# Performance work log

Measured on AMD Instinct MI355X. Metric: run time of the kernel, lower is better.

## Reference

```python
import jax, jax.numpy as jnp
import numpy as np

SCALE = 32.0 / 32.0  # alpha / rank
KEEP = 1.0 - 0.05    # dropout keep prob


def setup_inputs() -> dict:
    key = jax.random.key(0)
    kx, kw, ka, kb, km = jax.random.split(key, 5)
    B_, S, D_in, D_out, R = 4, 2048, 4096, 4096, 32
    x = jax.random.normal(kx, (B_, S, D_in), dtype=jnp.float32)
    W = jax.random.normal(kw, (D_out, D_in), dtype=jnp.float32) * (1.0 / np.sqrt(D_in))
    A = jax.random.normal(ka, (D_in, R), dtype=jnp.float32) * (1.0 / np.sqrt(D_in))
    Bm = jax.random.normal(kb, (R, D_out), dtype=jnp.float32) * 0.02
    # deterministic inverted-dropout mask: {0, 1/KEEP}
    drop_mask = (jax.random.uniform(km, (B_, S, D_in)) < KEEP).astype(jnp.float32) / KEEP
    return {"x": x, "W": W, "A": A, "B": Bm, "drop_mask": drop_mask}


def reference(x, W, A, B, drop_mask):
    # base: F.linear(x, W)  -> x @ W.T   [b,s,out]
    base = jnp.einsum("bsi,oi->bso", x, W)
    # lora: dropout(x) @ A @ B, low-rank path (contract rank first)
    lora = jnp.einsum("bsr,ro->bso", jnp.einsum("bsi,ir->bsr", x * drop_mask, A), B)
    return base + SCALE * lora
```

## Files before the change

kernel.cpp:

```cpp
#include <hip/hip_runtime.h>
#include <hip/hip_bf16.h>

typedef short bf16x8 __attribute__((ext_vector_type(8)));
typedef float f32x4  __attribute__((ext_vector_type(4)));

#define DIN  4096
#define DOUT 4096
#define MTOT 8192
#define RNK  32
#define NT   64

union Pk8 { __hip_bfloat16 h[8]; uint4 u; bf16x8 v; };

__device__ __forceinline__ uint4 pack8(float a0,float a1,float a2,float a3,
                                       float b0,float b1,float b2,float b3){
  Pk8 p;
  p.h[0]=__float2bfloat16(a0); p.h[1]=__float2bfloat16(a1);
  p.h[2]=__float2bfloat16(a2); p.h[3]=__float2bfloat16(a3);
  p.h[4]=__float2bfloat16(b0); p.h[5]=__float2bfloat16(b1);
  p.h[6]=__float2bfloat16(b2); p.h[7]=__float2bfloat16(b3);
  return p.u;
}
__device__ __forceinline__ bf16x8 pack8v(float a0,float a1,float a2,float a3,
                                         float b0,float b1,float b2,float b3){
  Pk8 p;
  p.h[0]=__float2bfloat16(a0); p.h[1]=__float2bfloat16(a1);
  p.h[2]=__float2bfloat16(a2); p.h[3]=__float2bfloat16(a3);
  p.h[4]=__float2bfloat16(b0); p.h[5]=__float2bfloat16(b1);
  p.h[6]=__float2bfloat16(b2); p.h[7]=__float2bfloat16(b3);
  return p.v;
}

__device__ __forceinline__ void gload_lds16(const void* g, void* l){
  __builtin_amdgcn_global_load_lds(
      (const __attribute__((address_space(1))) unsigned int*)g,
      (__attribute__((address_space(3))) unsigned int*)l, 16, 0, 0);
}

#define MFMA(A,B,C) __builtin_amdgcn_mfma_f32_16x16x32_bf16(A,B,C,0,0,0)
#define BAR   asm volatile("s_barrier" ::: "memory")
#define SB0   __builtin_amdgcn_sched_barrier(0)
#define PRIO1 __builtin_amdgcn_s_setprio(1)
#define PRIO0 __builtin_amdgcn_s_setprio(0)

__global__ __launch_bounds__(256) void k_conv_w(const float* __restrict__ W,
                                                __hip_bfloat16* __restrict__ Wb){
  size_t i = ((size_t)blockIdx.x*256 + threadIdx.x) * 8;
  float4 a = *(const float4*)(W + i);
  float4 b = *(const float4*)(W + i + 4);
  *(uint4*)(Wb + i) = pack8(a.x,a.y,a.z,a.w,b.x,b.y,b.z,b.w);
}

__global__ __launch_bounds__(256) void k_conv_ab(const float* __restrict__ A,
                                                 const float* __restrict__ B,
                                                 __hip_bfloat16* __restrict__ At,
                                                 __hip_bfloat16* __restrict__ Bt){
  int idx = blockIdx.x*256 + threadIdx.x;
  if (idx < DIN*RNK){
    int k = idx >> 5, r = idx & 31;
    At[(size_t)r*DIN + k] = __float2bfloat16(A[(size_t)k*RNK + r]);
  } else {
    int j = idx - DIN*RNK;
    int n = j >> 5, k = j & 31;
    Bt[(size_t)n*RNK + k] = __float2bfloat16(B[(size_t)k*DOUT + n]);
  }
}

__global__ __launch_bounds__(256) void k_xt(const float* __restrict__ x,
                                            const float* __restrict__ mk,
                                            const __hip_bfloat16* __restrict__ At,
                                            __hip_bfloat16* __restrict__ xb,
                                            __hip_bfloat16* __restrict__ tb){
  __shared__ float sred[4*512];
  const int t = threadIdx.x, w = t >> 6, l = t & 63;
  const int r0 = blockIdx.x * 16;
  const int lane15 = l & 15, kb = l >> 4;
  const size_t rowbase = (size_t)(r0 + lane15) * DIN;
  const int kbase = w * 1024;

  f32x4 acc0 = {0.f,0.f,0.f,0.f}, acc1 = {0.f,0.f,0.f,0.f};
  const __hip_bfloat16* at0 = At + (size_t)lane15*DIN;
  const __hip_bfloat16* at1 = At + (size_t)(16+lane15)*DIN;

  #pragma unroll 2
  for (int kt = 0; kt < 32; ++kt){
    const int k0 = kbase + kt*32 + kb*8;
    float4 xa = *(const float4*)(x  + rowbase + k0);
    float4 xc = *(const float4*)(x  + rowbase + k0 + 4);
    float4 ma = *(const float4*)(mk + rowbase + k0);
    float4 mc = *(const float4*)(mk + rowbase + k0 + 4);
    *(uint4*)(xb + rowbase + k0) = pack8(xa.x,xa.y,xa.z,xa.w,xc.x,xc.y,xc.z,xc.w);
    bf16x8 af = pack8v(xa.x*ma.x,xa.y*ma.y,xa.z*ma.z,xa.w*ma.w,
                       xc.x*mc.x,xc.y*mc.y,xc.z*mc.z,xc.w*mc.w);
    bf16x8 b0 = *(const bf16x8*)(at0 + k0);
    bf16x8 b1 = *(const bf16x8*)(at1 + k0);
    acc0 = MFMA(af, b0, acc0);
    acc1 = MFMA(af, b1, acc1);
  }

  #pragma unroll
  for (int r = 0; r < 4; ++r){
    sred[(w*64+l)*8 + r]     = acc0[r];
    sred[(w*64+l)*8 + 4 + r] = acc1[r];
  }
  __syncthreads();
  #pragma unroll
  for (int e2 = 0; e2 < 2; ++e2){
    int e  = t*2 + e2;
    int el = e >> 3, er = e & 7;
    float s = sred[el*8+er] + sred[512+el*8+er] + sred[1024+el*8+er] + sred[1536+el*8+er];
    int col  = (er>>2)*16 + (el & 15);
    int orow = (el>>4)*4 + (er & 3);
    tb[(size_t)(r0 + orow)*RNK + col] = __float2bfloat16(s);
  }
}

__global__ __launch_bounds__(512, 2) void k_main2(const __hip_bfloat16* __restrict__ xb,
                                                  const __hip_bfloat16* __restrict__ Wb,
                                                  const __hip_bfloat16* __restrict__ tb,
                                                  const __hip_bfloat16* __restrict__ Bt,
                                                  float* __restrict__ out){
  __shared__ __align__(16) __hip_bfloat16 lds[65536];
  const int tid = threadIdx.x;
  const int l  = tid & 63, w = tid >> 6;
  const int wm = w >> 2,  wn = w & 3;
  const int lr = l & 15;
  const int ch = ((l >> 4) ^ ((l >> 1) & 3)) & 3;
  const int laneA = (wm*128 + lr)*32 + ch*8;
  const int laneB = (wn*64  + lr)*32 + ch*8;
  const int g_row = tid >> 2;
  const int g_ch  = (((tid & 3) ^ ((tid >> 3) & 3))) * 8;

  const int bid  = blockIdx.x;
  const int xcd  = bid & 7;
  const int idx  = bid >> 3;
  const int bm0  = (((xcd >> 1) << 3) + (idx & 7)) * 256;
  const int bn0  = (((xcd & 1) << 3) + (idx >> 3)) * 256;

  f32x4 acc[8][4];

  {
    const __hip_bfloat16* tp = tb + (size_t)(bm0 + wm*128 + lr)*RNK + (l>>4)*8;
    const __hip_bfloat16* bp = Bt + (size_t)(bn0 + wn*64  + lr)*RNK + (l>>4)*8;
    bf16x8 tf[8], bf[4];
    #pragma unroll
    for (int m = 0; m < 8; ++m) tf[m] = *(const bf16x8*)(tp + m*16*RNK);
    #pragma unroll
    for (int n = 0; n < 4; ++n) bf[n] = *(const bf16x8*)(bp + n*16*RNK);
    const f32x4 z = {0.f,0.f,0.f,0.f};
    #pragma unroll
    for (int m = 0; m < 8; ++m)
      #pragma unroll
      for (int n = 0; n < 4; ++n)
        acc[m][n] = MFMA(tf[m], bf[n], z);
  }
  asm volatile("" ::: "memory");

  auto STAGE = [&](int bb, int ab, int kh, int kt){
    const __hip_bfloat16* g = ab ? Wb : xb;
    const int base0 = ab ? bn0 : bm0;
    const int segb  = bb*32768 + ab*16384 + kh*8192;
    #pragma unroll
    for (int i = 0; i < 2; ++i){
      const __hip_bfloat16* src = g + (size_t)(base0 + i*128 + g_row)*DIN
                                    + kt*64 + kh*32 + g_ch;
      gload_lds16(src, (void*)&lds[segb + i*4096 + w*512]);
    }
  };

  #define ASEG(bb,kh) ((bb)*32768 + (kh)*8192)
  #define BSEG(bb,kh) ((bb)*32768 + 16384 + (kh)*8192)
  #define LDV(off) (*(const bf16x8*)&lds[(off)])

  STAGE(0,1,0,0); STAGE(0,0,0,0); STAGE(0,1,1,0); STAGE(0,0,1,0);
  STAGE(1,1,0,1); STAGE(1,0,0,1); STAGE(1,1,1,1); STAGE(1,0,1,1);
  asm volatile("s_waitcnt vmcnt(8)" ::: "memory");
  BAR; SB0;

  bf16x8 aE[4], aO[4], bk0[4], bk1[4];
  #pragma unroll
  for (int i = 0; i < 4; ++i) aE[i] = LDV(ASEG(0,0)+laneA+i*512);
  #pragma unroll
  for (int n = 0; n < 4; ++n) bk0[n] = LDV(BSEG(0,0)+laneB+n*512);

  for (int t = 0; t < NT; ++t){
    const int b = t & 1, bn = b ^ 1;

    BAR; SB0;
    #pragma unroll
    for (int i = 0; i < 4; ++i) aO[i] = LDV(ASEG(b,0)+laneA+2048+i*512);
    #pragma unroll
    for (int n = 0; n < 4; ++n) bk1[n] = LDV(BSEG(b,1)+laneB+n*512);
    if (t+2 < NT) STAGE(b, 1, 0, t+2);
    PRIO1;
    #pragma unroll
    for (int n = 0; n < 4; ++n){
      acc[0][n] = MFMA(aE[0], bk0[n], acc[0][n]);
      acc[1][n] = MFMA(aE[1], bk0[n], acc[1][n]);
      acc[2][n] = MFMA(aE[2], bk0[n], acc[2][n]);
      acc[3][n] = MFMA(aE[3], bk0[n], acc[3][n]);
    }
    PRIO0;

    BAR; SB0;
    #pragma unroll
    for (int i = 0; i < 4; ++i) aE[i] = LDV(ASEG(b,1)+laneA+i*512);
    if (t+2 < NT) STAGE(b, 0, 0, t+2);
    PRIO1;
    #pragma unroll
    for (int n = 0; n < 4; ++n){
      acc[4][n] = MFMA(aO[0], bk0[n], acc[4][n]);
      acc[5][n] = MFMA(aO[1], bk0[n], acc[5][n]);
      acc[6][n] = MFMA(aO[2], bk0[n], acc[6][n]);
      acc[7][n] = MFMA(aO[3], bk0[n], acc[7][n]);
    }
    PRIO0;

    BAR; SB0;
    #pragma unroll
    for (int i = 0; i < 4; ++i) aO[i] = LDV(ASEG(b,1)+laneA+2048+i*512);
    if (t+2 < NT) STAGE(b, 1, 1, t+2);
    PRIO1;
    #pragma unroll
    for (int n = 0; n < 4; ++n){
      acc[0][n] = MFMA(aE[0], bk1[n], acc[0][n]);
      acc[1][n] = MFMA(aE[1], bk1[n], acc[1][n]);
      acc[2][n] = MFMA(aE[2], bk1[n], acc[2][n]);
      acc[3][n] = MFMA(aE[3], bk1[n], acc[3][n]);
    }
    PRIO0;
    asm volatile("s_waitcnt vmcnt(6)" ::: "memory");

    BAR; SB0;
    if (t+1 < NT){
      #pragma unroll
      for (int i = 0; i < 4; ++i) aE[i] = LDV(ASEG(bn,0)+laneA+i*512);
      #pragma unroll
      for (int n = 0; n < 4; ++n) bk0[n] = LDV(BSEG(bn,0)+laneB+n*512);
    }
    if (t+2 < NT) STAGE(b, 0, 1, t+2);
    PRIO1;
    #pragma unroll
    for (int n = 0; n < 4; ++n){
      acc[4][n] = MFMA(aO[0], bk1[n], acc[4][n]);
      acc[5][n] = MFMA(aO[1], bk1[n], acc[5][n]);
      acc[6][n] = MFMA(aO[2], bk1[n], acc[6][n]);
      acc[7][n] = MFMA(aO[3], bk1[n], acc[7][n]);
    }
    PRIO0;
  }

  const int orow = bm0 + wm*128 + (l>>4)*4;
  const int ocol = bn0 + wn*64  + (l&15);
  #pragma unroll
  for (int m = 0; m < 8; ++m)
    #pragma unroll
    for (int n = 0; n < 4; ++n)
      #pragma unroll
      for (int r = 0; r < 4; ++r)
        out[(size_t)(orow + m*16 + r)*DOUT + ocol + n*16] = acc[m][n][r];
  #undef LDV
  #undef ASEG
  #undef BSEG
}

__global__ void fb_t(const float* __restrict__ x, const float* __restrict__ mk,
                     const float* __restrict__ A, float* __restrict__ tf){
  const int m = blockIdx.x, t = threadIdx.x;
  float acc[RNK];
  #pragma unroll
  for (int r = 0; r < RNK; ++r) acc[r] = 0.f;
  for (int k = t; k < DIN; k += 256){
    float xm = x[(size_t)m*DIN + k] * mk[(size_t)m*DIN + k];
    #pragma unroll
    for (int r = 0; r < RNK; ++r) acc[r] += xm * A[(size_t)k*RNK + r];
  }
  #pragma unroll
  for (int r = 0; r < RNK; ++r){
    float v = acc[r];
    for (int o = 32; o; o >>= 1) v += __shfl_down(v, o);
    if ((t & 63) == 0) atomicAdd(&tf[(size_t)m*RNK + r], v);
  }
}

__global__ void fb_out(const float* __restrict__ x, const float* __restrict__ W,
                       const float* __restrict__ B, const float* __restrict__ tf,
                       float* __restrict__ out){
  size_t idx = (size_t)blockIdx.x*256 + threadIdx.x;
  int m = (int)(idx >> 12), n = (int)(idx & 4095);
  float acc = 0.f;
  for (int k = 0; k < DIN; ++k)
    acc += x[(size_t)m*DIN + k] * W[(size_t)n*DIN + k];
  #pragma unroll
  for (int r = 0; r < RNK; ++r)
    acc += tf[(size_t)m*RNK + r] * B[(size_t)r*DOUT + n];
  out[idx] = acc;
}

extern "C" void kernel_launch(void* const* d_in, const int* in_sizes, int n_in,
                              void* d_out, int out_size, void* d_ws, size_t ws_size,
                              hipStream_t stream) {
  const float* x  = (const float*)d_in[0];
  const float* W  = (const float*)d_in[1];
  const float* A  = (const float*)d_in[2];
  const float* B  = (const float*)d_in[3];
  const float* mk = (const float*)d_in[4];
  float* out = (float*)d_out;

  const size_t OFF_XB = 0;
  const size_t OFF_WB = OFF_XB + (size_t)MTOT*DIN*2;
  const size_t OFF_TB = OFF_WB + (size_t)DOUT*DIN*2;
  const size_t OFF_AT = OFF_TB + (size_t)MTOT*RNK*2;
  const size_t OFF_BT = OFF_AT + (size_t)RNK*DIN*2;
  const size_t NEED   = OFF_BT + (size_t)DIN*RNK*2;

  if (ws_size >= NEED){
    char* ws = (char*)d_ws;
    __hip_bfloat16* xb = (__hip_bfloat16*)(ws + OFF_XB);
    __hip_bfloat16* Wb = (__hip_bfloat16*)(ws + OFF_WB);
    __hip_bfloat16* tb = (__hip_bfloat16*)(ws + OFF_TB);
    __hip_bfloat16* At = (__hip_bfloat16*)(ws + OFF_AT);
    __hip_bfloat16* Bt = (__hip_bfloat16*)(ws + OFF_BT);

    k_conv_w <<<(DOUT*(size_t)DIN)/(256*8), 256, 0, stream>>>(W, Wb);
    k_conv_ab<<<(2*DIN*RNK)/256,            256, 0, stream>>>(A, B, At, Bt);
    k_xt     <<<MTOT/16,                    256, 0, stream>>>(x, mk, At, xb, tb);
    k_main2  <<<(MTOT/256)*(DOUT/256),      512, 0, stream>>>(xb, Wb, tb, Bt, out);
  } else {
    float* tf = (float*)d_ws;
    hipMemsetAsync(tf, 0, (size_t)MTOT*RNK*4, stream);
    fb_t  <<<MTOT, 256, 0, stream>>>(x, mk, A, tf);
    fb_out<<<((size_t)MTOT*DOUT)/256, 256, 0, stream>>>(x, W, B, tf, out);
  }
}
```

Baseline: 337.2 us.

## Switch main GEMM to 32x32x16 MFMA tiles and reorder LDS staging

Replaces the 16x16x32 bf16 MFMA tiling with 32x32x16 MFMAs, so each wave holds 4x2 accumulators of 16 floats instead of 8x4 of 4. LDS fragment addressing is rewritten for the 32-row layout with a new XOR swizzle. The prefetch schedule also changes: one stage of the next buffer is issued inside the loop rather than in the prologue, and the wait counts are adjusted. The larger MFMA is meant to cut LDS reads per FLOP and improve MFMA throughput, at the risk of new LDS bank conflicts and a more fragile pipeline.

```diff
diff --git a/kernel.cpp b/kernel.cpp
--- a/kernel.cpp
+++ b/kernel.cpp
@@ -3,6 +3,7 @@
 
 typedef short bf16x8 __attribute__((ext_vector_type(8)));
 typedef float f32x4  __attribute__((ext_vector_type(4)));
+typedef float f32x16 __attribute__((ext_vector_type(16)));
 
 #define DIN  4096
 #define DOUT 4096
@@ -37,7 +38,8 @@
       (__attribute__((address_space(3))) unsigned int*)l, 16, 0, 0);
 }
 
-#define MFMA(A,B,C) __builtin_amdgcn_mfma_f32_16x16x32_bf16(A,B,C,0,0,0)
+#define MFMA(A,B,C)   __builtin_amdgcn_mfma_f32_16x16x32_bf16(A,B,C,0,0,0)
+#define MFMA32(A,B,C) __builtin_amdgcn_mfma_f32_32x32x16_bf16(A,B,C,0,0,0)
 #define BAR   asm volatile("s_barrier" ::: "memory")
 #define SB0   __builtin_amdgcn_sched_barrier(0)
 #define PRIO1 __builtin_amdgcn_s_setprio(1)
@@ -115,7 +117,7 @@
   }
 }
 
-__global__ __launch_bounds__(512, 2) void k_main2(const __hip_bfloat16* __restrict__ xb,
+__global__ __launch_bounds__(512, 2) void k_main5(const __hip_bfloat16* __restrict__ xb,
                                                   const __hip_bfloat16* __restrict__ Wb,
                                                   const __hip_bfloat16* __restrict__ tb,
                                                   const __hip_bfloat16* __restrict__ Bt,
@@ -124,10 +126,12 @@
   const int tid = threadIdx.x;
   const int l  = tid & 63, w = tid >> 6;
   const int wm = w >> 2,  wn = w & 3;
-  const int lr = l & 15;
-  const int ch = ((l >> 4) ^ ((l >> 1) & 3)) & 3;
-  const int laneA = (wm*128 + lr)*32 + ch*8;
-  const int laneB = (wn*64  + lr)*32 + ch*8;
+  const int l31 = l & 31, kg = l >> 5;
+  const int swz = (l31 >> 1) & 3;
+  const int ck0 = ((kg)     ^ swz) * 8;
+  const int ck1 = ((2 + kg) ^ swz) * 8;
+  const int laneA = (wm*128 + l31)*32;
+  const int laneB = (wn*64  + l31)*32;
   const int g_row = tid >> 2;
   const int g_ch  = (((tid & 3) ^ ((tid >> 3) & 3))) * 8;
 
@@ -137,22 +141,30 @@
   const int bm0  = (((xcd >> 1) << 3) + (idx & 7)) * 256;
   const int bn0  = (((xcd & 1) << 3) + (idx >> 3)) * 256;
 
-  f32x4 acc[8][4];
+  f32x16 acc[4][2];
 
   {
-    const __hip_bfloat16* tp = tb + (size_t)(bm0 + wm*128 + lr)*RNK + (l>>4)*8;
-    const __hip_bfloat16* bp = Bt + (size_t)(bn0 + wn*64  + lr)*RNK + (l>>4)*8;
-    bf16x8 tf[8], bf[4];
-    #pragma unroll
-    for (int m = 0; m < 8; ++m) tf[m] = *(const bf16x8*)(tp + m*16*RNK);
-    #pragma unroll
-    for (int n = 0; n < 4; ++n) bf[n] = *(const bf16x8*)(bp + n*16*RNK);
-    const f32x4 z = {0.f,0.f,0.f,0.f};
-    #pragma unroll
-    for (int m = 0; m < 8; ++m)
-      #pragma unroll
-      for (int n = 0; n < 4; ++n)
-        acc[m][n] = MFMA(tf[m], bf[n], z);
+    const __hip_bfloat16* tp = tb + (size_t)(bm0 + wm*128 + l31)*RNK + kg*8;
+    const __hip_bfloat16* bp = Bt + (size_t)(bn0 + wn*64  + l31)*RNK + kg*8;
+    bf16x8 tf[4][2], bf[2][2];
+    #pragma unroll
+    for (int mf = 0; mf < 4; ++mf)
+      #pragma unroll
+      for (int s = 0; s < 2; ++s)
+        tf[mf][s] = *(const bf16x8*)(tp + (size_t)mf*32*RNK + s*16);
+    #pragma unroll
+    for (int nf = 0; nf < 2; ++nf)
+      #pragma unroll
+      for (int s = 0; s < 2; ++s)
+        bf[nf][s] = *(const bf16x8*)(bp + (size_t)nf*32*RNK + s*16);
+    const f32x16 z = {0.f,0.f,0.f,0.f,0.f,0.f,0.f,0.f,
+                      0.f,0.f,0.f,0.f,0.f,0.f,0.f,0.f};
+    #pragma unroll
+    for (int mf = 0; mf < 4; ++mf)
+      #pragma unroll
+      for (int nf = 0; nf < 2; ++nf)
+        acc[mf][nf] = MFMA32(tf[mf][1], bf[nf][1],
+                       MFMA32(tf[mf][0], bf[nf][0], z));
   }
   asm volatile("" ::: "memory");
 
@@ -173,92 +185,119 @@
   #define LDV(off) (*(const bf16x8*)&lds[(off)])
 
   STAGE(0,1,0,0); STAGE(0,0,0,0); STAGE(0,1,1,0); STAGE(0,0,1,0);
-  STAGE(1,1,0,1); STAGE(1,0,0,1); STAGE(1,1,1,1); STAGE(1,0,1,1);
-  asm volatile("s_waitcnt vmcnt(8)" ::: "memory");
+  STAGE(1,1,0,1); STAGE(1,0,0,1); STAGE(1,1,1,1);
+  asm volatile("s_waitcnt vmcnt(6)" ::: "memory");
   BAR; SB0;
 
-  bf16x8 aE[4], aO[4], bk0[4], bk1[4];
-  #pragma unroll
-  for (int i = 0; i < 4; ++i) aE[i] = LDV(ASEG(0,0)+laneA+i*512);
-  #pragma unroll
-  for (int n = 0; n < 4; ++n) bk0[n] = LDV(BSEG(0,0)+laneB+n*512);
+  bf16x8 aE[2][2], aO[2][2], bk0[2][2], bk1[2][2];
+  #pragma unroll
+  for (int m = 0; m < 2; ++m){
+    aE[m][0] = LDV(ASEG(0,0) + laneA + m*1024 + ck0);
+    aE[m][1] = LDV(ASEG(0,0) + laneA + m*1024 + ck1);
+  }
+  #pragma unroll
+  for (int n = 0; n < 2; ++n){
+    bk0[n][0] = LDV(BSEG(0,0) + laneB + n*1024 + ck0);
+    bk0[n][1] = LDV(BSEG(0,0) + laneB + n*1024 + ck1);
+  }
 
   for (int t = 0; t < NT; ++t){
     const int b = t & 1, bn = b ^ 1;
 
     BAR; SB0;
     #pragma unroll
-    for (int i = 0; i < 4; ++i) aO[i] = LDV(ASEG(b,0)+laneA+2048+i*512);
-    #pragma unroll
-    for (int n = 0; n < 4; ++n) bk1[n] = LDV(BSEG(b,1)+laneB+n*512);
+    for (int m = 0; m < 2; ++m){
+      aO[m][0] = LDV(ASEG(b,0) + laneA + (2+m)*1024 + ck0);
+      aO[m][1] = LDV(ASEG(b,0) + laneA + (2+m)*1024 + ck1);
+    }
+    #pragma unroll
+    for (int n = 0; n < 2; ++n){
+      bk1[n][0] = LDV(BSEG(b,1) + laneB + n*1024 + ck0);
+      bk1[n][1] = LDV(BSEG(b,1) + laneB + n*1024 + ck1);
+    }
+    if (t+1 < NT) STAGE(bn, 0, 1, t+1);
+    PRIO1;
+    #pragma unroll
+    for (int m = 0; m < 2; ++m)
+      #pragma unroll
+      for (int n = 0; n < 2; ++n){
+        acc[m][n] = MFMA32(aE[m][0], bk0[n][0], acc[m][n]);
+        acc[m][n] = MFMA32(aE[m][1], bk0[n][1], acc[m][n]);
+      }
+    PRIO0;
+
+    BAR; SB0;
+    #pragma unroll
+    for (int m = 0; m < 2; ++m){
+      aE[m][0] = LDV(ASEG(b,1) + laneA + m*1024 + ck0);
+      aE[m][1] = LDV(ASEG(b,1) + laneA + m*1024 + ck1);
+    }
     if (t+2 < NT) STAGE(b, 1, 0, t+2);
     PRIO1;
     #pragma unroll
-    for (int n = 0; n < 4; ++n){
-      acc[0][n] = MFMA(aE[0], bk0[n], acc[0][n]);
-      acc[1][n] = MFMA(aE[1], bk0[n], acc[1][n]);
-      acc[2][n] = MFMA(aE[2], bk0[n], acc[2][n]);
-      acc[3][n] = MFMA(aE[3], bk0[n], acc[3][n]);
-    }
+    for (int m = 0; m < 2; ++m)
+      #pragma unroll
+      for (int n = 0; n < 2; ++n){
+        acc[2+m][n] = MFMA32(aO[m][0], bk0[n][0], acc[2+m][n]);
+        acc[2+m][n] = MFMA32(aO[m][1], bk0[n][1], acc[2+m][n]);
+      }
     PRIO0;
 
     BAR; SB0;
     #pragma unroll
-    for (int i = 0; i < 4; ++i) aE[i] = LDV(ASEG(b,1)+laneA+i*512);
+    for (int m = 0; m < 2; ++m){
+      aO[m][0] = LDV(ASEG(b,1) + laneA + (2+m)*1024 + ck0);
+      aO[m][1] = LDV(ASEG(b,1) + laneA + (2+m)*1024 + ck1);
+    }
     if (t+2 < NT) STAGE(b, 0, 0, t+2);
     PRIO1;
     #pragma unroll
-    for (int n = 0; n < 4; ++n){
-      acc[4][n] = MFMA(aO[0], bk0[n], acc[4][n]);
-      acc[5][n] = MFMA(aO[1], bk0[n], acc[5][n]);
-      acc[6][n] = MFMA(aO[2], bk0[n], acc[6][n]);
-      acc[7][n] = MFMA(aO[3], bk0[n], acc[7][n]);
-    }
+    for (int m = 0; m < 2; ++m)
+      #pragma unroll
+      for (int n = 0; n < 2; ++n){
+        acc[m][n] = MFMA32(aE[m][0], bk1[n][0], acc[m][n]);
+        acc[m][n] = MFMA32(aE[m][1], bk1[n][1], acc[m][n]);
+      }
     PRIO0;
+    if (t < NT-2) asm volatile("s_waitcnt vmcnt(6)" ::: "memory");
+    else          asm volatile("s_waitcnt vmcnt(0)" ::: "memory");
 
     BAR; SB0;
-    #pragma unroll
-    for (int i = 0; i < 4; ++i) aO[i] = LDV(ASEG(b,1)+laneA+2048+i*512);
+    if (t+1 < NT){
+      #pragma unroll
+      for (int m = 0; m < 2; ++m){
+        aE[m][0] = LDV(ASEG(bn,0) + laneA + m*1024 + ck0);
+        aE[m][1] = LDV(ASEG(bn,0) + laneA + m*1024 + ck1);
+      }
+      #pragma unroll
+      for (int n = 0; n < 2; ++n){
+        bk0[n][0] = LDV(BSEG(bn,0) + laneB + n*1024 + ck0);
+        bk0[n][1] = LDV(BSEG(bn,0) + laneB + n*1024 + ck1);
+      }
+    }
     if (t+2 < NT) STAGE(b, 1, 1, t+2);
     PRIO1;
     #pragma unroll
-    for (int n = 0; n < 4; ++n){
-      acc[0][n] = MFMA(aE[0], bk1[n], acc[0][n]);
-      acc[1][n] = MFMA(aE[1], bk1[n], acc[1][n]);
-      acc[2][n] = MFMA(aE[2], bk1[n], acc[2][n]);
-      acc[3][n] = MFMA(aE[3], bk1[n], acc[3][n]);
-    }
+    for (int m = 0; m < 2; ++m)
+      #pragma unroll
+      for (int n = 0; n < 2; ++n){
+        acc[2+m][n] = MFMA32(aO[m][0], bk1[n][0], acc[2+m][n]);
+        acc[2+m][n] = MFMA32(aO[m][1], bk1[n][1], acc[2+m][n]);
+      }
     PRIO0;
-    asm volatile("s_waitcnt vmcnt(6)" ::: "memory");
-
-    BAR; SB0;
-    if (t+1 < NT){
-      #pragma unroll
-      for (int i = 0; i < 4; ++i) aE[i] = LDV(ASEG(bn,0)+laneA+i*512);
-      #pragma unroll
-      for (int n = 0; n < 4; ++n) bk0[n] = LDV(BSEG(bn,0)+laneB+n*512);
-    }
-    if (t+2 < NT) STAGE(b, 0, 1, t+2);
-    PRIO1;
-    #pragma unroll
-    for (int n = 0; n < 4; ++n){
-      acc[4][n] = MFMA(aO[0], bk1[n], acc[4][n]);
-      acc[5][n] = MFMA(aO[1], bk1[n], acc[5][n]);
-      acc[6][n] = MFMA(aO[2], bk1[n], acc[6][n]);
-      acc[7][n] = MFMA(aO[3], bk1[n], acc[7][n]);
-    }
-    PRIO0;
-  }
-
-  const int orow = bm0 + wm*128 + (l>>4)*4;
-  const int ocol = bn0 + wn*64  + (l&15);
-  #pragma unroll
-  for (int m = 0; m < 8; ++m)
-    #pragma unroll
-    for (int n = 0; n < 4; ++n)
-      #pragma unroll
-      for (int r = 0; r < 4; ++r)
-        out[(size_t)(orow + m*16 + r)*DOUT + ocol + n*16] = acc[m][n][r];
+    if (t < NT-2) asm volatile("s_waitcnt vmcnt(6)" ::: "memory");
+  }
+
+  const int orow = bm0 + wm*128 + 4*kg;
+  const int ocol = bn0 + wn*64  + l31;
+  #pragma unroll
+  for (int mf = 0; mf < 4; ++mf)
+    #pragma unroll
+    for (int nf = 0; nf < 2; ++nf)
+      #pragma unroll
+      for (int r = 0; r < 16; ++r)
+        out[(size_t)(orow + mf*32 + (r&3) + 8*(r>>2))*DOUT + ocol + nf*32]
+            = acc[mf][nf][r];
   #undef LDV
   #undef ASEG
   #undef BSEG
@@ -325,7 +364,7 @@
     k_conv_w <<<(DOUT*(size_t)DIN)/(256*8), 256, 0, stream>>>(W, Wb);
     k_conv_ab<<<(2*DIN*RNK)/256,            256, 0, stream>>>(A, B, At, Bt);
     k_xt     <<<MTOT/16,                    256, 0, stream>>>(x, mk, At, xb, tb);
-    k_main2  <<<(MTOT/256)*(DOUT/256),      512, 0, stream>>>(xb, Wb, tb, Bt, out);
+    k_main5  <<<(MTOT/256)*(DOUT/256),      512, 0, stream>>>(xb, Wb, tb, Bt, out);
   } else {
     float* tf = (float*)d_ws;
     hipMemsetAsync(tf, 0, (size_t)MTOT*RNK*4, stream);
```

Measured after the change: 355.5 us. +5.4%, slower.

## Restructure main GEMM loop into two half-K phases with full-tile MFMA blocks

Applied to the files above, without the earlier changes.

The inner loop of the bf16 GEMM changes from four quarter-phases (half of the M fragments each) to two phases per K-tile. Each phase loads all eight A fragments and four B fragments for one 32-wide K half, then issues 32 MFMAs. This halves the barriers per iteration and regroups the async global-to-LDS staging and vmcnt waits, with special-cased waits near the end. It raises register pressure (16 A fragments live) and drops the occupancy hint of 2 blocks per CU from launch_bounds, which could cost occupancy or cause spills.

```diff
diff --git a/kernel.cpp b/kernel.cpp
--- a/kernel.cpp
+++ b/kernel.cpp
@@ -115,17 +115,17 @@
   }
 }
 
-__global__ __launch_bounds__(512, 2) void k_main2(const __hip_bfloat16* __restrict__ xb,
-                                                  const __hip_bfloat16* __restrict__ Wb,
-                                                  const __hip_bfloat16* __restrict__ tb,
-                                                  const __hip_bfloat16* __restrict__ Bt,
-                                                  float* __restrict__ out){
+__global__ __launch_bounds__(512) void k_main7(const __hip_bfloat16* __restrict__ xb,
+                                               const __hip_bfloat16* __restrict__ Wb,
+                                               const __hip_bfloat16* __restrict__ tb,
+                                               const __hip_bfloat16* __restrict__ Bt,
+                                               float* __restrict__ out){
   __shared__ __align__(16) __hip_bfloat16 lds[65536];
   const int tid = threadIdx.x;
   const int l  = tid & 63, w = tid >> 6;
   const int wm = w >> 2,  wn = w & 3;
-  const int lr = l & 15;
-  const int ch = ((l >> 4) ^ ((l >> 1) & 3)) & 3;
+  const int lr = l & 15,  kb = l >> 4;
+  const int ch = (kb ^ ((l >> 1) & 3)) & 3;
   const int laneA = (wm*128 + lr)*32 + ch*8;
   const int laneB = (wn*64  + lr)*32 + ch*8;
   const int g_row = tid >> 2;
@@ -140,8 +140,8 @@
   f32x4 acc[8][4];
 
   {
-    const __hip_bfloat16* tp = tb + (size_t)(bm0 + wm*128 + lr)*RNK + (l>>4)*8;
-    const __hip_bfloat16* bp = Bt + (size_t)(bn0 + wn*64  + lr)*RNK + (l>>4)*8;
+    const __hip_bfloat16* tp = tb + (size_t)(bm0 + wm*128 + lr)*RNK + kb*8;
+    const __hip_bfloat16* bp = Bt + (size_t)(bn0 + wn*64  + lr)*RNK + kb*8;
     bf16x8 tf[8], bf[4];
     #pragma unroll
     for (int m = 0; m < 8; ++m) tf[m] = *(const bf16x8*)(tp + m*16*RNK);
@@ -172,82 +172,54 @@
   #define BSEG(bb,kh) ((bb)*32768 + 16384 + (kh)*8192)
   #define LDV(off) (*(const bf16x8*)&lds[(off)])
 
-  STAGE(0,1,0,0); STAGE(0,0,0,0); STAGE(0,1,1,0); STAGE(0,0,1,0);
-  STAGE(1,1,0,1); STAGE(1,0,0,1); STAGE(1,1,1,1); STAGE(1,0,1,1);
+  STAGE(0,0,0,0); STAGE(0,1,0,0); STAGE(0,0,1,0); STAGE(0,1,1,0);
+  STAGE(1,0,0,1); STAGE(1,1,0,1);
+  STAGE(1,0,1,1); STAGE(1,1,1,1);
   asm volatile("s_waitcnt vmcnt(8)" ::: "memory");
   BAR; SB0;
 
-  bf16x8 aE[4], aO[4], bk0[4], bk1[4];
-  #pragma unroll
-  for (int i = 0; i < 4; ++i) aE[i] = LDV(ASEG(0,0)+laneA+i*512);
-  #pragma unroll
-  for (int n = 0; n < 4; ++n) bk0[n] = LDV(BSEG(0,0)+laneB+n*512);
+  bf16x8 aF[8], aS[8], bF[4], bS[4];
+  #pragma unroll
+  for (int m = 0; m < 8; ++m) aF[m] = LDV(ASEG(0,0) + laneA + m*512);
+  #pragma unroll
+  for (int n = 0; n < 4; ++n) bF[n] = LDV(BSEG(0,0) + laneB + n*512);
 
   for (int t = 0; t < NT; ++t){
-    const int b = t & 1, bn = b ^ 1;
+    const int b = t & 1, bo = b ^ 1;
 
     BAR; SB0;
     #pragma unroll
-    for (int i = 0; i < 4; ++i) aO[i] = LDV(ASEG(b,0)+laneA+2048+i*512);
-    #pragma unroll
-    for (int n = 0; n < 4; ++n) bk1[n] = LDV(BSEG(b,1)+laneB+n*512);
-    if (t+2 < NT) STAGE(b, 1, 0, t+2);
+    for (int m = 0; m < 8; ++m) aS[m] = LDV(ASEG(b,1) + laneA + m*512);
+    #pragma unroll
+    for (int n = 0; n < 4; ++n) bS[n] = LDV(BSEG(b,1) + laneB + n*512);
+    if (t+2 < NT){ STAGE(b,0,0,t+2); STAGE(b,1,0,t+2); }
     PRIO1;
     #pragma unroll
-    for (int n = 0; n < 4; ++n){
-      acc[0][n] = MFMA(aE[0], bk0[n], acc[0][n]);
-      acc[1][n] = MFMA(aE[1], bk0[n], acc[1][n]);
-      acc[2][n] = MFMA(aE[2], bk0[n], acc[2][n]);
-      acc[3][n] = MFMA(aE[3], bk0[n], acc[3][n]);
-    }
+    for (int m = 0; m < 8; ++m)
+      #pragma unroll
+      for (int n = 0; n < 4; ++n)
+        acc[m][n] = MFMA(aF[m], bF[n], acc[m][n]);
     PRIO0;
-
-    BAR; SB0;
-    #pragma unroll
-    for (int i = 0; i < 4; ++i) aE[i] = LDV(ASEG(b,1)+laneA+i*512);
-    if (t+2 < NT) STAGE(b, 0, 0, t+2);
-    PRIO1;
-    #pragma unroll
-    for (int n = 0; n < 4; ++n){
-      acc[4][n] = MFMA(aO[0], bk0[n], acc[4][n]);
-      acc[5][n] = MFMA(aO[1], bk0[n], acc[5][n]);
-      acc[6][n] = MFMA(aO[2], bk0[n], acc[6][n]);
-      acc[7][n] = MFMA(aO[3], bk0[n], acc[7][n]);
-    }
-    PRIO0;
-
-    BAR; SB0;
-    #pragma unroll
-    for (int i = 0; i < 4; ++i) aO[i] = LDV(ASEG(b,1)+laneA+2048+i*512);
-    if (t+2 < NT) STAGE(b, 1, 1, t+2);
-    PRIO1;
-    #pragma unroll
-    for (int n = 0; n < 4; ++n){
-      acc[0][n] = MFMA(aE[0], bk1[n], acc[0][n]);
-      acc[1][n] = MFMA(aE[1], bk1[n], acc[1][n]);
-      acc[2][n] = MFMA(aE[2], bk1[n], acc[2][n]);
-      acc[3][n] = MFMA(aE[3], bk1[n], acc[3][n]);
-    }
-    PRIO0;
-    asm volatile("s_waitcnt vmcnt(6)" ::: "memory");
+    if (t < NT-2)       asm volatile("s_waitcnt vmcnt(8)" ::: "memory");
+    else if (t == NT-2) asm volatile("s_waitcnt vmcnt(4)" ::: "memory");
 
     BAR; SB0;
     if (t+1 < NT){
       #pragma unroll
-      for (int i = 0; i < 4; ++i) aE[i] = LDV(ASEG(bn,0)+laneA+i*512);
-      #pragma unroll
-      for (int n = 0; n < 4; ++n) bk0[n] = LDV(BSEG(bn,0)+laneB+n*512);
+      for (int m = 0; m < 8; ++m) aF[m] = LDV(ASEG(bo,0) + laneA + m*512);
+      #pragma unroll
+      for (int n = 0; n < 4; ++n) bF[n] = LDV(BSEG(bo,0) + laneB + n*512);
     }
-    if (t+2 < NT) STAGE(b, 0, 1, t+2);
+    if (t+2 < NT){ STAGE(b,0,1,t+2); STAGE(b,1,1,t+2); }
     PRIO1;
     #pragma unroll
-    for (int n = 0; n < 4; ++n){
-      acc[4][n] = MFMA(aO[0], bk1[n], acc[4][n]);
-      acc[5][n] = MFMA(aO[1], bk1[n], acc[5][n]);
-      acc[6][n] = MFMA(aO[2], bk1[n], acc[6][n]);
-      acc[7][n] = MFMA(aO[3], bk1[n], acc[7][n]);
-    }
+    for (int m = 0; m < 8; ++m)
+      #pragma unroll
+      for (int n = 0; n < 4; ++n)
+        acc[m][n] = MFMA(aS[m], bS[n], acc[m][n]);
     PRIO0;
+    if (t < NT-2)       asm volatile("s_waitcnt vmcnt(8)" ::: "memory");
+    else if (t == NT-2) asm volatile("s_waitcnt vmcnt(0)" ::: "memory");
   }
 
   const int orow = bm0 + wm*128 + (l>>4)*4;
@@ -325,7 +297,7 @@
     k_conv_w <<<(DOUT*(size_t)DIN)/(256*8), 256, 0, stream>>>(W, Wb);
     k_conv_ab<<<(2*DIN*RNK)/256,            256, 0, stream>>>(A, B, At, Bt);
     k_xt     <<<MTOT/16,                    256, 0, stream>>>(x, mk, At, xb, tb);
-    k_main2  <<<(MTOT/256)*(DOUT/256),      512, 0, stream>>>(xb, Wb, tb, Bt, out);
+    k_main7  <<<(MTOT/256)*(DOUT/256),      512, 0, stream>>>(xb, Wb, tb, Bt, out);
   } else {
     float* tf = (float*)d_ws;
     hipMemsetAsync(tf, 0, (size_t)MTOT*RNK*4, stream);
```

Result: slower. 358.7 us (+6.4%).
